# Performance work log

Hardware: AMD Instinct MI355X
Metric: run time of the kernel (lower is better)

The kernel has to match this reference:

```python
import jax, jax.numpy as jnp
import numpy as np

B, S, DM, H = 4, 1024, 1024, 16
D = DM // H  # head size 64


def setup_inputs() -> dict:
    key = jax.random.key(0)
    ks = jax.random.split(key, 8)
    scale = 1.0 / np.sqrt(DM)
    return {
        "hidden_states": jax.random.normal(ks[0], (B, S, DM), dtype=jnp.float32),
        "attention_mask": jnp.zeros((B, 1, 1, S), dtype=jnp.float32),
        "link_mask": jax.random.uniform(ks[1], (B, 1, S, S), dtype=jnp.float32),
        "Wq": jax.random.normal(ks[2], (DM, DM), dtype=jnp.float32) * scale,
        "bq": jnp.zeros((DM,), dtype=jnp.float32),
        "Wk": jax.random.normal(ks[3], (DM, DM), dtype=jnp.float32) * scale,
        "bk": jnp.zeros((DM,), dtype=jnp.float32),
        "Wv": jax.random.normal(ks[4], (DM, DM), dtype=jnp.float32) * scale,
        "bv": jnp.zeros((DM,), dtype=jnp.float32),
    }


def _split_heads(x):
    # [B,S,DM] -> [B,H,S,D]
    return x.reshape(B, S, H, D).transpose(0, 2, 1, 3)


def reference(hidden_states, attention_mask, link_mask, Wq, bq, Wk, bk, Wv, bv):
    q = _split_heads(hidden_states @ Wq.T + bq)
    k = _split_heads(hidden_states @ Wk.T + bk)
    v = _split_heads(hidden_states @ Wv.T + bv)
    # [B,H,S,S]
    scores = jnp.einsum("bhqd,bhkd->bhqk", q, k) / jnp.float32(np.sqrt(D))
    scores = scores + attention_mask  # additive mask, broadcast [B,1,1,S]
    probs = jax.nn.softmax(scores, axis=-1)
    # post-softmax multiplicative link mask (un-normalizes rows)
    probs = probs * link_mask
    # dropout prob 0.0 (eval) -> identity
    ctx = jnp.einsum("bhqk,bhkd->bhqd", probs, v)
    ctx = ctx.transpose(0, 2, 1, 3).reshape(B, S, DM)
    return ctx
```

## Files before the change

kernel.cpp:

```cpp
#include <hip/hip_runtime.h>
#include <hip/hip_bf16.h>
#include <cstdint>

typedef __attribute__((ext_vector_type(8))) __bf16 bf16x8;
typedef __attribute__((ext_vector_type(4))) float f32x4;
typedef unsigned short u16;
typedef unsigned int u32;

struct alignas(8) U16x4 { u16 x, y, z, w; };
struct alignas(8) U32x2 { u32 x, y; };

__device__ __forceinline__ u16 f2b(float x) {
    u32 u = __builtin_bit_cast(u32, x);
    u += 0x7fffu + ((u >> 16) & 1u);
    return (u16)(u >> 16);
}
__device__ __forceinline__ u32 cvtpk(float lo, float hi) {
    u32 r;
    asm("v_cvt_pk_bf16_f32 %0, %1, %2" : "=v"(r) : "v"(lo), "v"(hi));
    return r;
}
__device__ __forceinline__ float vexp2(float x) {
    float r;
    asm("v_exp_f32 %0, %1" : "=v"(r) : "v"(x));
    return r;
}

#define LOG2E 1.44269504088896f

__global__ __launch_bounds__(256) void cvt_kernel(
    const float* __restrict__ hs,
    const float* __restrict__ wq, const float* __restrict__ wk, const float* __restrict__ wv,
    const float* __restrict__ amask,
    u16* __restrict__ hsb, u16* __restrict__ wb, float* __restrict__ amask2)
{
    if (blockIdx.x == 7168) {
        int t = threadIdx.x;
        #pragma unroll
        for (int j = 0; j < 4; ++j) {
            float4 v = ((const float4*)amask)[t + j * 256];
            v.x *= LOG2E; v.y *= LOG2E; v.z *= LOG2E; v.w *= LOG2E;
            ((float4*)amask2)[t + j * 256] = v;
        }
        return;
    }
    int i = blockIdx.x * 256 + threadIdx.x;
    const float4* src; u16* dst; int off;
    if (i < 1048576) { src = (const float4*)hs; dst = hsb; off = i; }
    else {
        int j = i - 1048576;
        int w = j >> 18;
        int o = j & 262143;
        src = (const float4*)(w == 0 ? wq : (w == 1 ? wk : wv));
        dst = wb + w * 1048576;
        off = o;
    }
    float4 v = src[off];
    U16x4 r; r.x = f2b(v.x); r.y = f2b(v.y); r.z = f2b(v.z); r.w = f2b(v.w);
    *(U16x4*)(dst + off * 4) = r;
}

__global__ __launch_bounds__(256, 3) void qkv_gemm(
    const u16* __restrict__ A, const u16* __restrict__ W,
    const float* __restrict__ bq, const float* __restrict__ bk, const float* __restrict__ bv,
    u16* __restrict__ Qo, u16* __restrict__ Ko, u16* __restrict__ Vt)
{
    __shared__ u16 As[2][128 * 32];
    __shared__ u16 Bs[2][128 * 32];
    const int tid = threadIdx.x;
    const int lane = tid & 63, wid = tid >> 6;
    const int wr = (wid >> 1) * 64, wc = (wid & 1) * 64;
    const int g = lane >> 4, c = lane & 15;

    int lin = blockIdx.y * 24 + blockIdx.x;
    int wg = (lin & 7) * 96 + (lin >> 3);
    const int bn = wg >> 5;
    const int bm = wg & 31;

    f32x4 acc[4][4] = {};

#define GSTAGE(bf, k0)                                                              \
    {                                                                               \
        _Pragma("unroll") for (int i = 0; i < 2; ++i) {                             \
            int chunk = i * 256 + tid;                                              \
            int row = chunk >> 2, col = (chunk & 3) * 8;                            \
            const u16* ga = A + (bm * 128 + row) * 1024 + (k0) + col;               \
            const u16* gb = W + (bn * 128 + row) * 1024 + (k0) + col;               \
            u16* la = &As[bf][0] + (i * 256 + wid * 64) * 8;                        \
            u16* lb = &Bs[bf][0] + (i * 256 + wid * 64) * 8;                        \
            __builtin_amdgcn_global_load_lds((const __attribute__((address_space(1))) u32*)ga, \
                                             (__attribute__((address_space(3))) u32*)la, 16, 0, 0); \
            __builtin_amdgcn_global_load_lds((const __attribute__((address_space(1))) u32*)gb, \
                                             (__attribute__((address_space(3))) u32*)lb, 16, 0, 0); \
        }                                                                           \
    }

    GSTAGE(0, 0);

    int cur = 0;
    for (int t = 0; t < 32; ++t) {
        __syncthreads();
        if (t < 31) GSTAGE(cur ^ 1, (t + 1) * 32);
        bf16x8 af[4], bf4[4];
        #pragma unroll
        for (int i = 0; i < 4; ++i)
            af[i] = *(const bf16x8*)(&As[cur][0] + (wr + i * 16 + c) * 32 + g * 8);
        #pragma unroll
        for (int j = 0; j < 4; ++j)
            bf4[j] = *(const bf16x8*)(&Bs[cur][0] + (wc + j * 16 + c) * 32 + g * 8);
        #pragma unroll
        for (int i = 0; i < 4; ++i)
            #pragma unroll
            for (int j = 0; j < 4; ++j)
                acc[i][j] = __builtin_amdgcn_mfma_f32_16x16x32_bf16(af[i], bf4[j], acc[i][j], 0, 0, 0);
        cur ^= 1;
    }
#undef GSTAGE

    const int region = bn >> 3;
    const float* bias = region == 0 ? bq : (region == 1 ? bk : bv);
    #pragma unroll
    for (int i = 0; i < 4; ++i) {
        int m0 = bm * 128 + wr + i * 16 + g * 4;
        int b = m0 >> 10, s0 = m0 & 1023;
        #pragma unroll
        for (int j = 0; j < 4; ++j) {
            int n = (bn & 7) * 128 + wc + j * 16 + c;
            float bb = bias[n];
            int h = n >> 6, d = n & 63;
            int bh = b * 16 + h;
            if (region == 2) {
                U16x4 pk;
                pk.x = f2b(acc[i][j][0] + bb);
                pk.y = f2b(acc[i][j][1] + bb);
                pk.z = f2b(acc[i][j][2] + bb);
                pk.w = f2b(acc[i][j][3] + bb);
                *(U16x4*)(Vt + (bh * 64 + d) * 1024 + s0) = pk;
            } else if (region == 1) {
                #pragma unroll
                for (int r = 0; r < 4; ++r)
                    Ko[(bh * 1024 + s0 + r) * 64 + d] = f2b(acc[i][j][r] + bb);
            } else {
                #pragma unroll
                for (int r = 0; r < 4; ++r)
                    Qo[(bh * 1024 + s0 + r) * 64 + d] = f2b((acc[i][j][r] + bb) * (0.125f * LOG2E));
            }
        }
    }
}

__global__ __launch_bounds__(256, 4) void attn_kernel(
    const u16* __restrict__ Q, const u16* __restrict__ K, const u16* __restrict__ Vt,
    const float* __restrict__ amask, const float* __restrict__ link,
    float* __restrict__ out)
{
    __shared__ u16 Ks[2][32 * 64];
    __shared__ u16 Vs[2][64 * 32];
    __shared__ float Ls[2][64 * 32];
    __shared__ u16 P[4][16 * 32];
    const int tid = threadIdx.x;
    const int lane = tid & 63, wid = tid >> 6;
    const int g = lane >> 4, c = lane & 15;
    const int c7 = c & 7;
    const int s2 = (c >> 1) & 3;

    int hw = blockIdx.x;
    int logical = (hw & 7) * 128 + (hw >> 3);
    int b = logical >> 8;
    int qt = (logical >> 4) & 15;
    int h = logical & 15;
    int bh = b * 16 + h;
    const int qbase = qt * 64 + wid * 16;

    const u16* Qh = Q + bh * 65536;
    const u16* Kh = K + bh * 65536;
    const u16* Vh = Vt + bh * 65536;
    const float* Lq = link + (size_t)b * 1048576 + (size_t)(qt * 64) * 1024;

    bf16x8 qfx0 = *(const bf16x8*)(Qh + (qbase + c) * 64 + g * 8);
    bf16x8 qfx1 = *(const bf16x8*)(Qh + (qbase + c) * 64 + 32 + g * 8);

    float lsum = 0.f;
    f32x4 ctx[4] = {};
    u16* const Pb = &P[wid][0];

    const int krow = tid >> 3, kcir = (tid & 7) ^ (krow & 7);
    const int vrow = tid >> 2, vcir = (tid & 3) ^ ((vrow >> 1) & 3);
    const int lr1i = (256 + tid) >> 3;
    const int lc1 = ((256 + tid) & 7) ^ (lr1i & 7);
    const u16* gk   = Kh + krow * 64 + kcir * 8;
    const u16* gv   = Vh + vrow * 1024 + vcir * 8;
    const float* gl0 = Lq + krow * 1024 + kcir * 4;
    const float* gl1 = Lq + lr1i * 1024 + lc1 * 4;
    const float* mkP = amask + b * 1024;

#define AS3(p) (__attribute__((address_space(3))) u32*)(p)
#define AS1(p) (const __attribute__((address_space(1))) u32*)(p)
#define ISSUE_STAGE(B)                                                              \
    {                                                                               \
        __builtin_amdgcn_global_load_lds(AS1(gk),  AS3(&Ks[B][0] + wid * 512), 16, 0, 0); \
        __builtin_amdgcn_global_load_lds(AS1(gv),  AS3(&Vs[B][0] + wid * 512), 16, 0, 0); \
        __builtin_amdgcn_global_load_lds(AS1(gl0), AS3(&Ls[B][0] + wid * 256), 16, 0, 0); \
        __builtin_amdgcn_global_load_lds(AS1(gl1), AS3(&Ls[B][0] + 1024 + wid * 256), 16, 0, 0); \
        gk += 2048; gv += 32; gl0 += 32; gl1 += 32;                                 \
    }

#define ATILE(B, T)                                                                 \
    {                                                                               \
        __syncthreads();                 \
        if ((T) < 31) ISSUE_STAGE((B) ^ 1)                                          \
        _Pragma("unroll") for (int kt = 0; kt < 2; ++kt) {                          \
            bf16x8 kf0 = *(const bf16x8*)(&Ks[B][0] + (kt * 16 + c) * 64 + ((g)     ^ c7) * 8); \
            bf16x8 kf1 = *(const bf16x8*)(&Ks[B][0] + (kt * 16 + c) * 64 + ((4 + g) ^ c7) * 8); \
            f32x4 sc = {};                                                          \
            sc = __builtin_amdgcn_mfma_f32_16x16x32_bf16(kf0, qfx0, sc, 0, 0, 0);   \
            sc = __builtin_amdgcn_mfma_f32_16x16x32_bf16(kf1, qfx1, sc, 0, 0, 0);   \
            f32x4 m4  = *(const f32x4*)(mkP + kt * 16 + g * 4);                     \
            f32x4 lk4 = *(const f32x4*)(&Ls[B][0] + (wid * 16 + c) * 32 + ((kt * 4 + g) ^ c7) * 4); \
            float e0 = vexp2(sc[0] + m4[0]);                                        \
            float e1 = vexp2(sc[1] + m4[1]);                                        \
            float e2 = vexp2(sc[2] + m4[2]);                                        \
            float e3 = vexp2(sc[3] + m4[3]);                                        \
            lsum += (e0 + e1) + (e2 + e3);                                          \
            U32x2 pw;                                                               \
            pw.x = cvtpk(e0 * lk4[0], e1 * lk4[1]);                                 \
            pw.y = cvtpk(e2 * lk4[2], e3 * lk4[3]);                                 \
            *(U32x2*)(Pb + c * 32 + (((kt * 4 + g) ^ (s2 << 1)) * 4)) = pw;         \
        }                                                                           \
        __builtin_amdgcn_s_setprio(1);                                              \
        bf16x8 pf = *(const bf16x8*)(Pb + c * 32 + ((g ^ s2) * 8));                 \
        _Pragma("unroll") for (int dt = 0; dt < 4; ++dt) {                          \
            bf16x8 vf = *(const bf16x8*)(&Vs[B][0] + (dt * 16 + c) * 32 + ((g ^ s2) * 8)); \
            ctx[dt] = __builtin_amdgcn_mfma_f32_16x16x32_bf16(pf, vf, ctx[dt], 0, 0, 0); \
        }                                                                           \
        __builtin_amdgcn_s_setprio(0);                                              \
        mkP += 32;                                                                  \
    }

    ISSUE_STAGE(0)

    for (int it = 0; it < 16; ++it) {
        ATILE(0, it * 2);
        ATILE(1, it * 2 + 1);
    }
#undef ATILE
#undef ISSUE_STAGE
#undef AS3
#undef AS1

    lsum += __shfl_xor(lsum, 16, 64);
    lsum += __shfl_xor(lsum, 32, 64);

    #pragma unroll
    for (int r = 0; r < 4; ++r) {
        float inv = 1.0f / __shfl(lsum, g * 4 + r, 16);
        int q = qbase + g * 4 + r;
        float* orow = out + (size_t)b * 1048576 + (size_t)q * 1024 + h * 64;
        #pragma unroll
        for (int dt = 0; dt < 4; ++dt)
            orow[dt * 16 + c] = ctx[dt][r] * inv;
    }
}

extern "C" void kernel_launch(void* const* d_in, const int* in_sizes, int n_in,
                              void* d_out, int out_size, void* d_ws, size_t ws_size,
                              hipStream_t stream)
{
    (void)in_sizes; (void)n_in; (void)out_size; (void)ws_size;
    const float* hs    = (const float*)d_in[0];
    const float* amask = (const float*)d_in[1];
    const float* link  = (const float*)d_in[2];
    const float* Wq    = (const float*)d_in[3];
    const float* bq    = (const float*)d_in[4];
    const float* Wk    = (const float*)d_in[5];
    const float* bk    = (const float*)d_in[6];
    const float* Wv    = (const float*)d_in[7];
    const float* bv    = (const float*)d_in[8];
    float* out = (float*)d_out;

    char* ws = (char*)d_ws;
    u16* hsb = (u16*)ws;
    u16* wb  = (u16*)(ws + (8u  << 20));
    u16* Qb  = (u16*)(ws + (14u << 20));
    u16* Kb  = (u16*)(ws + (22u << 20));
    u16* Vtb = (u16*)(ws + (30u << 20));
    float* amask2 = (float*)(ws + (38u << 20));

    cvt_kernel<<<7169, 256, 0, stream>>>(hs, Wq, Wk, Wv, amask, hsb, wb, amask2);
    qkv_gemm<<<dim3(24, 32), 256, 0, stream>>>(hsb, wb, bq, bk, bv, Qb, Kb, Vtb);
    attn_kernel<<<1024, 256, 0, stream>>>(Qb, Kb, Vtb, amask2, link, out);
}
```

Before: 86.79 us.

## Switch attention to 32x32 MFMA tiles with register-resident P via permlane swap

The attention kernel now gives each wave 32 query rows instead of 16 and uses 32x32x16 bf16 MFMAs for both QK^T and PV. The probability tile is repacked in registers with v_permlane32_swap rather than round-tripping through LDS. This drops the P shared buffer and its LDS traffic, and the 32-row softmax sums reduce with a single shuffle. In exchange the block count halves to 512, occupancy drops to 2 blocks per CU, and each block stages twice as much link-mask data.

```diff
diff --git a/kernel.cpp b/kernel.cpp
--- a/kernel.cpp
+++ b/kernel.cpp
@@ -4,11 +4,12 @@
 
 typedef __attribute__((ext_vector_type(8))) __bf16 bf16x8;
 typedef __attribute__((ext_vector_type(4))) float f32x4;
+typedef __attribute__((ext_vector_type(16))) float f32x16;
 typedef unsigned short u16;
 typedef unsigned int u32;
 
 struct alignas(8) U16x4 { u16 x, y, z, w; };
-struct alignas(8) U32x2 { u32 x, y; };
+struct alignas(16) U32x4 { u32 x, y, z, w; };
 
 __device__ __forceinline__ u16 f2b(float x) {
     u32 u = __builtin_bit_cast(u32, x);
@@ -24,6 +25,9 @@
     float r;
     asm("v_exp_f32 %0, %1" : "=v"(r) : "v"(x));
     return r;
+}
+__device__ __forceinline__ void plswap(u32& a, u32& b) {
+    asm("v_permlane32_swap_b32 %0, %1" : "+v"(a), "+v"(b));
 }
 
 #define LOG2E 1.44269504088896f
@@ -149,50 +153,52 @@
     }
 }
 
-__global__ __launch_bounds__(256, 4) void attn_kernel(
+__global__ __launch_bounds__(256, 2) void attn_kernel(
     const u16* __restrict__ Q, const u16* __restrict__ K, const u16* __restrict__ Vt,
     const float* __restrict__ amask, const float* __restrict__ link,
     float* __restrict__ out)
 {
     __shared__ u16 Ks[2][32 * 64];
     __shared__ u16 Vs[2][64 * 32];
-    __shared__ float Ls[2][64 * 32];
-    __shared__ u16 P[4][16 * 32];
+    __shared__ float Ls[2][128 * 32];
     const int tid = threadIdx.x;
     const int lane = tid & 63, wid = tid >> 6;
-    const int g = lane >> 4, c = lane & 15;
-    const int c7 = c & 7;
-    const int s2 = (c >> 1) & 3;
+    const int c5 = lane & 31, hi = lane >> 5;
+    const int c7 = c5 & 7;
+    const int s2 = (c5 >> 1) & 3;
 
     int hw = blockIdx.x;
-    int logical = (hw & 7) * 128 + (hw >> 3);
-    int b = logical >> 8;
-    int qt = (logical >> 4) & 15;
+    int logical = (hw & 7) * 64 + (hw >> 3);
+    int b = logical >> 7;
+    int qt = (logical >> 4) & 7;
     int h = logical & 15;
     int bh = b * 16 + h;
-    const int qbase = qt * 64 + wid * 16;
+    const int qbase = qt * 128 + wid * 32;
 
     const u16* Qh = Q + bh * 65536;
     const u16* Kh = K + bh * 65536;
     const u16* Vh = Vt + bh * 65536;
-    const float* Lq = link + (size_t)b * 1048576 + (size_t)(qt * 64) * 1024;
-
-    bf16x8 qfx0 = *(const bf16x8*)(Qh + (qbase + c) * 64 + g * 8);
-    bf16x8 qfx1 = *(const bf16x8*)(Qh + (qbase + c) * 64 + 32 + g * 8);
+    const float* mkP = amask + b * 1024;
+    const float* Lq = link + (size_t)b * 1048576 + (size_t)(qt * 128) * 1024;
+
+    bf16x8 qf[4];
+    #pragma unroll
+    for (int m = 0; m < 4; ++m)
+        qf[m] = *(const bf16x8*)(Qh + (qbase + c5) * 64 + m * 16 + hi * 8);
 
     float lsum = 0.f;
-    f32x4 ctx[4] = {};
-    u16* const Pb = &P[wid][0];
-
-    const int krow = tid >> 3, kcir = (tid & 7) ^ (krow & 7);
-    const int vrow = tid >> 2, vcir = (tid & 3) ^ ((vrow >> 1) & 3);
-    const int lr1i = (256 + tid) >> 3;
-    const int lc1 = ((256 + tid) & 7) ^ (lr1i & 7);
-    const u16* gk   = Kh + krow * 64 + kcir * 8;
-    const u16* gv   = Vh + vrow * 1024 + vcir * 8;
-    const float* gl0 = Lq + krow * 1024 + kcir * 4;
-    const float* gl1 = Lq + lr1i * 1024 + lc1 * 4;
-    const float* mkP = amask + b * 1024;
+    f32x16 ctx0 = {}, ctx1 = {};
+
+    const int krow = tid >> 3;
+    const int vrow = tid >> 2;
+    const int lrow = tid >> 3;
+    const u16* gk  = Kh + krow * 64 + (((tid & 7) ^ (krow & 7)) * 8);
+    const u16* gv  = Vh + vrow * 1024 + (((tid & 3) ^ ((vrow >> 1) & 3)) * 8);
+    const int lcir = (tid & 7) ^ (lrow & 7);
+    const float* gl0 = Lq + (lrow +  0) * 1024 + lcir * 4;
+    const float* gl1 = Lq + (lrow + 32) * 1024 + lcir * 4;
+    const float* gl2 = Lq + (lrow + 64) * 1024 + lcir * 4;
+    const float* gl3 = Lq + (lrow + 96) * 1024 + lcir * 4;
 
 #define AS3(p) (__attribute__((address_space(3))) u32*)(p)
 #define AS1(p) (const __attribute__((address_space(1))) u32*)(p)
@@ -200,38 +206,51 @@
     {                                                                               \
         __builtin_amdgcn_global_load_lds(AS1(gk),  AS3(&Ks[B][0] + wid * 512), 16, 0, 0); \
         __builtin_amdgcn_global_load_lds(AS1(gv),  AS3(&Vs[B][0] + wid * 512), 16, 0, 0); \
-        __builtin_amdgcn_global_load_lds(AS1(gl0), AS3(&Ls[B][0] + wid * 256), 16, 0, 0); \
+        __builtin_amdgcn_global_load_lds(AS1(gl0), AS3(&Ls[B][0] +        wid * 256), 16, 0, 0); \
         __builtin_amdgcn_global_load_lds(AS1(gl1), AS3(&Ls[B][0] + 1024 + wid * 256), 16, 0, 0); \
-        gk += 2048; gv += 32; gl0 += 32; gl1 += 32;                                 \
+        __builtin_amdgcn_global_load_lds(AS1(gl2), AS3(&Ls[B][0] + 2048 + wid * 256), 16, 0, 0); \
+        __builtin_amdgcn_global_load_lds(AS1(gl3), AS3(&Ls[B][0] + 3072 + wid * 256), 16, 0, 0); \
+        gk += 2048; gv += 32; gl0 += 32; gl1 += 32; gl2 += 32; gl3 += 32;           \
     }
 
 #define ATILE(B, T)                                                                 \
     {                                                                               \
         __syncthreads();                 \
         if ((T) < 31) ISSUE_STAGE((B) ^ 1)                                          \
-        _Pragma("unroll") for (int kt = 0; kt < 2; ++kt) {                          \
-            bf16x8 kf0 = *(const bf16x8*)(&Ks[B][0] + (kt * 16 + c) * 64 + ((g)     ^ c7) * 8); \
-            bf16x8 kf1 = *(const bf16x8*)(&Ks[B][0] + (kt * 16 + c) * 64 + ((4 + g) ^ c7) * 8); \
-            f32x4 sc = {};                                                          \
-            sc = __builtin_amdgcn_mfma_f32_16x16x32_bf16(kf0, qfx0, sc, 0, 0, 0);   \
-            sc = __builtin_amdgcn_mfma_f32_16x16x32_bf16(kf1, qfx1, sc, 0, 0, 0);   \
-            f32x4 m4  = *(const f32x4*)(mkP + kt * 16 + g * 4);                     \
-            f32x4 lk4 = *(const f32x4*)(&Ls[B][0] + (wid * 16 + c) * 32 + ((kt * 4 + g) ^ c7) * 4); \
-            float e0 = vexp2(sc[0] + m4[0]);                                        \
-            float e1 = vexp2(sc[1] + m4[1]);                                        \
-            float e2 = vexp2(sc[2] + m4[2]);                                        \
-            float e3 = vexp2(sc[3] + m4[3]);                                        \
-            lsum += (e0 + e1) + (e2 + e3);                                          \
-            U32x2 pw;                                                               \
-            pw.x = cvtpk(e0 * lk4[0], e1 * lk4[1]);                                 \
-            pw.y = cvtpk(e2 * lk4[2], e3 * lk4[3]);                                 \
-            *(U32x2*)(Pb + c * 32 + (((kt * 4 + g) ^ (s2 << 1)) * 4)) = pw;         \
-        }                                                                           \
+        f32x16 sc = {};                                                             \
+        _Pragma("unroll") for (int m = 0; m < 4; ++m) {                             \
+            bf16x8 kf = *(const bf16x8*)(&Ks[B][0] + c5 * 64 + (((2 * m + hi) ^ c7) * 8)); \
+            sc = __builtin_amdgcn_mfma_f32_32x32x16_bf16(kf, qf[m], sc, 0, 0, 0);   \
+        }                                                                           \
+        f32x4 mq[4], lq[4];                                                         \
+        _Pragma("unroll") for (int j = 0; j < 4; ++j) {                             \
+            mq[j] = *(const f32x4*)(mkP + j * 8 + hi * 4);                          \
+            lq[j] = *(const f32x4*)(&Ls[B][0] + (wid * 32 + c5) * 32 + (((2 * j + hi) ^ c7) * 4)); \
+        }                                                                           \
+        float p[16];                                                                \
+        _Pragma("unroll") for (int r = 0; r < 16; ++r) {                            \
+            float e = vexp2(sc[r] + mq[r >> 2][r & 3]);                             \
+            lsum += e;                                                              \
+            p[r] = e * lq[r >> 2][r & 3];                                           \
+        }                                                                           \
+        u32 a0 = cvtpk(p[0], p[1]),   b0 = cvtpk(p[4], p[5]);                       \
+        u32 a1 = cvtpk(p[2], p[3]),   b1 = cvtpk(p[6], p[7]);                       \
+        u32 a2 = cvtpk(p[8], p[9]),   b2 = cvtpk(p[12], p[13]);                     \
+        u32 a3 = cvtpk(p[10], p[11]), b3 = cvtpk(p[14], p[15]);                     \
+        plswap(a0, b0); plswap(a1, b1); plswap(a2, b2); plswap(a3, b3);             \
+        U32x4 w0 = {a0, a1, b0, b1}, w1 = {a2, a3, b2, b3};                         \
+        bf16x8 pa0 = __builtin_bit_cast(bf16x8, w0);           \
+        bf16x8 pa1 = __builtin_bit_cast(bf16x8, w1);           \
         __builtin_amdgcn_s_setprio(1);                                              \
-        bf16x8 pf = *(const bf16x8*)(Pb + c * 32 + ((g ^ s2) * 8));                 \
-        _Pragma("unroll") for (int dt = 0; dt < 4; ++dt) {                          \
-            bf16x8 vf = *(const bf16x8*)(&Vs[B][0] + (dt * 16 + c) * 32 + ((g ^ s2) * 8)); \
-            ctx[dt] = __builtin_amdgcn_mfma_f32_16x16x32_bf16(pf, vf, ctx[dt], 0, 0, 0); \
+        {                                                                           \
+            bf16x8 v00 = *(const bf16x8*)(&Vs[B][0] + c5 * 32 + (((0 + hi) ^ s2) * 8)); \
+            bf16x8 v01 = *(const bf16x8*)(&Vs[B][0] + c5 * 32 + (((2 + hi) ^ s2) * 8)); \
+            bf16x8 v10 = *(const bf16x8*)(&Vs[B][0] + (32 + c5) * 32 + (((0 + hi) ^ s2) * 8)); \
+            bf16x8 v11 = *(const bf16x8*)(&Vs[B][0] + (32 + c5) * 32 + (((2 + hi) ^ s2) * 8)); \
+            ctx0 = __builtin_amdgcn_mfma_f32_32x32x16_bf16(v00, pa0, ctx0, 0, 0, 0); \
+            ctx1 = __builtin_amdgcn_mfma_f32_32x32x16_bf16(v10, pa0, ctx1, 0, 0, 0); \
+            ctx0 = __builtin_amdgcn_mfma_f32_32x32x16_bf16(v01, pa1, ctx0, 0, 0, 0); \
+            ctx1 = __builtin_amdgcn_mfma_f32_32x32x16_bf16(v11, pa1, ctx1, 0, 0, 0); \
         }                                                                           \
         __builtin_amdgcn_s_setprio(0);                                              \
         mkP += 32;                                                                  \
@@ -248,17 +267,18 @@
 #undef AS3
 #undef AS1
 
-    lsum += __shfl_xor(lsum, 16, 64);
     lsum += __shfl_xor(lsum, 32, 64);
-
+    float inv = 1.0f / lsum;
+
+    float* orow = out + (size_t)b * 1048576 + (size_t)(qbase + c5) * 1024 + h * 64;
     #pragma unroll
-    for (int r = 0; r < 4; ++r) {
-        float inv = 1.0f / __shfl(lsum, g * 4 + r, 16);
-        int q = qbase + g * 4 + r;
-        float* orow = out + (size_t)b * 1048576 + (size_t)q * 1024 + h * 64;
-        #pragma unroll
-        for (int dt = 0; dt < 4; ++dt)
-            orow[dt * 16 + c] = ctx[dt][r] * inv;
+    for (int rq = 0; rq < 4; ++rq) {
+        f32x4 o0 = { ctx0[rq * 4 + 0] * inv, ctx0[rq * 4 + 1] * inv,
+                     ctx0[rq * 4 + 2] * inv, ctx0[rq * 4 + 3] * inv };
+        f32x4 o1 = { ctx1[rq * 4 + 0] * inv, ctx1[rq * 4 + 1] * inv,
+                     ctx1[rq * 4 + 2] * inv, ctx1[rq * 4 + 3] * inv };
+        *(f32x4*)(orow + rq * 8 + hi * 4)      = o0;
+        *(f32x4*)(orow + 32 + rq * 8 + hi * 4) = o1;
     }
 }
 
@@ -288,5 +308,5 @@
 
     cvt_kernel<<<7169, 256, 0, stream>>>(hs, Wq, Wk, Wv, amask, hsb, wb, amask2);
     qkv_gemm<<<dim3(24, 32), 256, 0, stream>>>(hsb, wb, bq, bk, bv, Qb, Kb, Vtb);
-    attn_kernel<<<1024, 256, 0, stream>>>(Qb, Kb, Vtb, amask2, link, out);
-}
+    attn_kernel<<<512, 256, 0, stream>>>(Qb, Kb, Vtb, amask2, link, out);
+}
```

Result: no change. 86.37 us (-0.5%).

## Double attention query tile per block to reuse K/V tiles across 32 rows per wave

Applied to the files above, without the earlier changes.

Each wave now handles 32 query rows instead of 16, so every block covers 128 queries and the grid shrinks from 1024 to 512 blocks. Each K and V tile loaded into shared memory now feeds twice as many MFMAs, which halves K/V global and LDS traffic per query. The link-mask staging buffer and P scratch double in size and the launch bound drops to 2 blocks per CU. The cost is higher register and LDS pressure, lower occupancy, and fewer blocks to spread across the CUs.

```diff
diff --git a/kernel.cpp b/kernel.cpp
--- a/kernel.cpp
+++ b/kernel.cpp
@@ -149,15 +149,15 @@
     }
 }
 
-__global__ __launch_bounds__(256, 4) void attn_kernel(
+__global__ __launch_bounds__(256, 2) void attn_kernel(
     const u16* __restrict__ Q, const u16* __restrict__ K, const u16* __restrict__ Vt,
     const float* __restrict__ amask, const float* __restrict__ link,
     float* __restrict__ out)
 {
     __shared__ u16 Ks[2][32 * 64];
     __shared__ u16 Vs[2][64 * 32];
-    __shared__ float Ls[2][64 * 32];
-    __shared__ u16 P[4][16 * 32];
+    __shared__ float Ls[2][128 * 32];
+    __shared__ u16 P[4][32 * 32];
     const int tid = threadIdx.x;
     const int lane = tid & 63, wid = tid >> 6;
     const int g = lane >> 4, c = lane & 15;
@@ -165,33 +165,37 @@
     const int s2 = (c >> 1) & 3;
 
     int hw = blockIdx.x;
-    int logical = (hw & 7) * 128 + (hw >> 3);
-    int b = logical >> 8;
-    int qt = (logical >> 4) & 15;
+    int logical = (hw & 7) * 64 + (hw >> 3);
+    int b = logical >> 7;
+    int qt = (logical >> 4) & 7;
     int h = logical & 15;
     int bh = b * 16 + h;
-    const int qbase = qt * 64 + wid * 16;
+    const int qbase = qt * 128 + wid * 32;
 
     const u16* Qh = Q + bh * 65536;
     const u16* Kh = K + bh * 65536;
     const u16* Vh = Vt + bh * 65536;
-    const float* Lq = link + (size_t)b * 1048576 + (size_t)(qt * 64) * 1024;
-
-    bf16x8 qfx0 = *(const bf16x8*)(Qh + (qbase + c) * 64 + g * 8);
-    bf16x8 qfx1 = *(const bf16x8*)(Qh + (qbase + c) * 64 + 32 + g * 8);
-
-    float lsum = 0.f;
-    f32x4 ctx[4] = {};
+    const float* Lq = link + (size_t)b * 1048576 + (size_t)(qt * 128) * 1024;
+
+    bf16x8 qf00 = *(const bf16x8*)(Qh + (qbase + c) * 64 + g * 8);
+    bf16x8 qf01 = *(const bf16x8*)(Qh + (qbase + c) * 64 + 32 + g * 8);
+    bf16x8 qf10 = *(const bf16x8*)(Qh + (qbase + 16 + c) * 64 + g * 8);
+    bf16x8 qf11 = *(const bf16x8*)(Qh + (qbase + 16 + c) * 64 + 32 + g * 8);
+
+    float lsum0 = 0.f, lsum1 = 0.f;
+    f32x4 ctx0[4] = {}, ctx1[4] = {};
     u16* const Pb = &P[wid][0];
 
     const int krow = tid >> 3, kcir = (tid & 7) ^ (krow & 7);
     const int vrow = tid >> 2, vcir = (tid & 3) ^ ((vrow >> 1) & 3);
-    const int lr1i = (256 + tid) >> 3;
-    const int lc1 = ((256 + tid) & 7) ^ (lr1i & 7);
+    const int lrow = tid >> 3;
+    const int lcir = (tid & 7) ^ (lrow & 7);
     const u16* gk   = Kh + krow * 64 + kcir * 8;
     const u16* gv   = Vh + vrow * 1024 + vcir * 8;
-    const float* gl0 = Lq + krow * 1024 + kcir * 4;
-    const float* gl1 = Lq + lr1i * 1024 + lc1 * 4;
+    const float* gl0 = Lq + (lrow +  0) * 1024 + lcir * 4;
+    const float* gl1 = Lq + (lrow + 32) * 1024 + lcir * 4;
+    const float* gl2 = Lq + (lrow + 64) * 1024 + lcir * 4;
+    const float* gl3 = Lq + (lrow + 96) * 1024 + lcir * 4;
     const float* mkP = amask + b * 1024;
 
 #define AS3(p) (__attribute__((address_space(3))) u32*)(p)
@@ -200,9 +204,11 @@
     {                                                                               \
         __builtin_amdgcn_global_load_lds(AS1(gk),  AS3(&Ks[B][0] + wid * 512), 16, 0, 0); \
         __builtin_amdgcn_global_load_lds(AS1(gv),  AS3(&Vs[B][0] + wid * 512), 16, 0, 0); \
-        __builtin_amdgcn_global_load_lds(AS1(gl0), AS3(&Ls[B][0] + wid * 256), 16, 0, 0); \
+        __builtin_amdgcn_global_load_lds(AS1(gl0), AS3(&Ls[B][0] +        wid * 256), 16, 0, 0); \
         __builtin_amdgcn_global_load_lds(AS1(gl1), AS3(&Ls[B][0] + 1024 + wid * 256), 16, 0, 0); \
-        gk += 2048; gv += 32; gl0 += 32; gl1 += 32;                                 \
+        __builtin_amdgcn_global_load_lds(AS1(gl2), AS3(&Ls[B][0] + 2048 + wid * 256), 16, 0, 0); \
+        __builtin_amdgcn_global_load_lds(AS1(gl3), AS3(&Ls[B][0] + 3072 + wid * 256), 16, 0, 0); \
+        gk += 2048; gv += 32; gl0 += 32; gl1 += 32; gl2 += 32; gl3 += 32;           \
     }
 
 #define ATILE(B, T)                                                                 \
@@ -212,26 +218,46 @@
         _Pragma("unroll") for (int kt = 0; kt < 2; ++kt) {                          \
             bf16x8 kf0 = *(const bf16x8*)(&Ks[B][0] + (kt * 16 + c) * 64 + ((g)     ^ c7) * 8); \
             bf16x8 kf1 = *(const bf16x8*)(&Ks[B][0] + (kt * 16 + c) * 64 + ((4 + g) ^ c7) * 8); \
-            f32x4 sc = {};                                                          \
-            sc = __builtin_amdgcn_mfma_f32_16x16x32_bf16(kf0, qfx0, sc, 0, 0, 0);   \
-            sc = __builtin_amdgcn_mfma_f32_16x16x32_bf16(kf1, qfx1, sc, 0, 0, 0);   \
-            f32x4 m4  = *(const f32x4*)(mkP + kt * 16 + g * 4);                     \
-            f32x4 lk4 = *(const f32x4*)(&Ls[B][0] + (wid * 16 + c) * 32 + ((kt * 4 + g) ^ c7) * 4); \
-            float e0 = vexp2(sc[0] + m4[0]);                                        \
-            float e1 = vexp2(sc[1] + m4[1]);                                        \
-            float e2 = vexp2(sc[2] + m4[2]);                                        \
-            float e3 = vexp2(sc[3] + m4[3]);                                        \
-            lsum += (e0 + e1) + (e2 + e3);                                          \
-            U32x2 pw;                                                               \
-            pw.x = cvtpk(e0 * lk4[0], e1 * lk4[1]);                                 \
-            pw.y = cvtpk(e2 * lk4[2], e3 * lk4[3]);                                 \
-            *(U32x2*)(Pb + c * 32 + (((kt * 4 + g) ^ (s2 << 1)) * 4)) = pw;         \
+            f32x4 sc0 = {}, sc1 = {};                                               \
+            sc0 = __builtin_amdgcn_mfma_f32_16x16x32_bf16(kf0, qf00, sc0, 0, 0, 0); \
+            sc0 = __builtin_amdgcn_mfma_f32_16x16x32_bf16(kf1, qf01, sc0, 0, 0, 0); \
+            sc1 = __builtin_amdgcn_mfma_f32_16x16x32_bf16(kf0, qf10, sc1, 0, 0, 0); \
+            sc1 = __builtin_amdgcn_mfma_f32_16x16x32_bf16(kf1, qf11, sc1, 0, 0, 0); \
+            f32x4 m4 = *(const f32x4*)(mkP + kt * 16 + g * 4);                      \
+            {                                                           \
+                f32x4 lk4 = *(const f32x4*)(&Ls[B][0] + (wid * 32 + c) * 32 + ((kt * 4 + g) ^ c7) * 4); \
+                float e0 = vexp2(sc0[0] + m4[0]);                                   \
+                float e1 = vexp2(sc0[1] + m4[1]);                                   \
+                float e2 = vexp2(sc0[2] + m4[2]);                                   \
+                float e3 = vexp2(sc0[3] + m4[3]);                                   \
+                lsum0 += (e0 + e1) + (e2 + e3);                                     \
+                U32x2 pw;                                                           \
+                pw.x = cvtpk(e0 * lk4[0], e1 * lk4[1]);                             \
+                pw.y = cvtpk(e2 * lk4[2], e3 * lk4[3]);                             \
+                *(U32x2*)(Pb + c * 32 + (((kt * 4 + g) ^ (s2 << 1)) * 4)) = pw;     \
+            }                                                                       \
+            {                                                           \
+                f32x4 lk4 = *(const f32x4*)(&Ls[B][0] + (wid * 32 + 16 + c) * 32 + ((kt * 4 + g) ^ c7) * 4); \
+                float e0 = vexp2(sc1[0] + m4[0]);                                   \
+                float e1 = vexp2(sc1[1] + m4[1]);                                   \
+                float e2 = vexp2(sc1[2] + m4[2]);                                   \
+                float e3 = vexp2(sc1[3] + m4[3]);                                   \
+                lsum1 += (e0 + e1) + (e2 + e3);                                     \
+                U32x2 pw;                                                           \
+                pw.x = cvtpk(e0 * lk4[0], e1 * lk4[1]);                             \
+                pw.y = cvtpk(e2 * lk4[2], e3 * lk4[3]);                             \
+                *(U32x2*)(Pb + (16 + c) * 32 + (((kt * 4 + g) ^ (s2 << 1)) * 4)) = pw; \
+            }                                                                       \
         }                                                                           \
         __builtin_amdgcn_s_setprio(1);                                              \
-        bf16x8 pf = *(const bf16x8*)(Pb + c * 32 + ((g ^ s2) * 8));                 \
-        _Pragma("unroll") for (int dt = 0; dt < 4; ++dt) {                          \
-            bf16x8 vf = *(const bf16x8*)(&Vs[B][0] + (dt * 16 + c) * 32 + ((g ^ s2) * 8)); \
-            ctx[dt] = __builtin_amdgcn_mfma_f32_16x16x32_bf16(pf, vf, ctx[dt], 0, 0, 0); \
+        {                                                                           \
+            bf16x8 pf0 = *(const bf16x8*)(Pb + c * 32 + ((g ^ s2) * 8));            \
+            bf16x8 pf1 = *(const bf16x8*)(Pb + (16 + c) * 32 + ((g ^ s2) * 8));     \
+            _Pragma("unroll") for (int dt = 0; dt < 4; ++dt) {                      \
+                bf16x8 vf = *(const bf16x8*)(&Vs[B][0] + (dt * 16 + c) * 32 + ((g ^ s2) * 8)); \
+                ctx0[dt] = __builtin_amdgcn_mfma_f32_16x16x32_bf16(pf0, vf, ctx0[dt], 0, 0, 0); \
+                ctx1[dt] = __builtin_amdgcn_mfma_f32_16x16x32_bf16(pf1, vf, ctx1[dt], 0, 0, 0); \
+            }                                                                       \
         }                                                                           \
         __builtin_amdgcn_s_setprio(0);                                              \
         mkP += 32;                                                                  \
@@ -248,17 +274,23 @@
 #undef AS3
 #undef AS1
 
-    lsum += __shfl_xor(lsum, 16, 64);
-    lsum += __shfl_xor(lsum, 32, 64);
+    lsum0 += __shfl_xor(lsum0, 16, 64);
+    lsum0 += __shfl_xor(lsum0, 32, 64);
+    lsum1 += __shfl_xor(lsum1, 16, 64);
+    lsum1 += __shfl_xor(lsum1, 32, 64);
 
     #pragma unroll
     for (int r = 0; r < 4; ++r) {
-        float inv = 1.0f / __shfl(lsum, g * 4 + r, 16);
-        int q = qbase + g * 4 + r;
-        float* orow = out + (size_t)b * 1048576 + (size_t)q * 1024 + h * 64;
-        #pragma unroll
-        for (int dt = 0; dt < 4; ++dt)
-            orow[dt * 16 + c] = ctx[dt][r] * inv;
+        float inv0 = 1.0f / __shfl(lsum0, g * 4 + r, 16);
+        float inv1 = 1.0f / __shfl(lsum1, g * 4 + r, 16);
+        int q0 = qbase + g * 4 + r;
+        float* orow0 = out + (size_t)b * 1048576 + (size_t)q0 * 1024 + h * 64;
+        float* orow1 = orow0 + 16 * 1024;
+        #pragma unroll
+        for (int dt = 0; dt < 4; ++dt) {
+            orow0[dt * 16 + c] = ctx0[dt][r] * inv0;
+            orow1[dt * 16 + c] = ctx1[dt][r] * inv1;
+        }
     }
 }
 
@@ -288,5 +320,5 @@
 
     cvt_kernel<<<7169, 256, 0, stream>>>(hs, Wq, Wk, Wv, amask, hsb, wb, amask2);
     qkv_gemm<<<dim3(24, 32), 256, 0, stream>>>(hsb, wb, bq, bk, bv, Qb, Kb, Vtb);
-    attn_kernel<<<1024, 256, 0, stream>>>(Qb, Kb, Vtb, amask2, link, out);
-}
+    attn_kernel<<<512, 256, 0, stream>>>(Qb, Kb, Vtb, amask2, link, out);
+}
```

Result: no change. 86.68 us (-0.1%).

## Pre-convert link mask to permuted bf16 and stream it into attention

Applied to the files above, without the earlier changes.

Adds a pass to the conversion kernel that turns the fp32 link mask into bf16. The pass also permutes each 32-column block to match the fragment order the attention kernel reads. The attention kernel then loads half as many link bytes per tile, with one async LDS copy instead of two, and unpacks bf16 pairs with shifts and masks. The cost being targeted is the repeated per-head reads of the full-precision link mask through cache and LDS. In exchange it adds an extra write and read of the converted buffer per call and rounds the mask to bf16 before the multiply.

```diff
diff --git a/kernel.cpp b/kernel.cpp
--- a/kernel.cpp
+++ b/kernel.cpp
@@ -9,6 +9,7 @@
 
 struct alignas(8) U16x4 { u16 x, y, z, w; };
 struct alignas(8) U32x2 { u32 x, y; };
+struct alignas(16) U32x4 { u32 x, y, z, w; };
 
 __device__ __forceinline__ u16 f2b(float x) {
     u32 u = __builtin_bit_cast(u32, x);
@@ -25,14 +26,19 @@
     asm("v_exp_f32 %0, %1" : "=v"(r) : "v"(x));
     return r;
 }
+__device__ __forceinline__ float blo(u32 w) { return __builtin_bit_cast(float, w << 16); }
+__device__ __forceinline__ float bhi(u32 w) { return __builtin_bit_cast(float, w & 0xffff0000u); }
 
 #define LOG2E 1.44269504088896f
+#define AS3(p) (__attribute__((address_space(3))) u32*)(p)
+#define AS1(p) (const __attribute__((address_space(1))) u32*)(p)
 
 __global__ __launch_bounds__(256) void cvt_kernel(
     const float* __restrict__ hs,
     const float* __restrict__ wq, const float* __restrict__ wk, const float* __restrict__ wv,
-    const float* __restrict__ amask,
-    u16* __restrict__ hsb, u16* __restrict__ wb, float* __restrict__ amask2)
+    const float* __restrict__ amask, const float* __restrict__ link,
+    u16* __restrict__ hsb, u16* __restrict__ wb, float* __restrict__ amask2,
+    u16* __restrict__ linkb)
 {
     if (blockIdx.x == 7168) {
         int t = threadIdx.x;
@@ -42,6 +48,17 @@
             v.x *= LOG2E; v.y *= LOG2E; v.z *= LOG2E; v.w *= LOG2E;
             ((float4*)amask2)[t + j * 256] = v;
         }
+        return;
+    }
+    if (blockIdx.x > 7168) {
+        int chunk = (blockIdx.x - 7169) * 256 + threadIdx.x;
+        float4 v = ((const float4*)link)[chunk];
+        int row = chunk >> 8;
+        int k4 = chunk & 255;
+        int blk = k4 >> 3, k4in = k4 & 7;
+        int newu = ((k4in & 3) << 1) | (k4in >> 2);
+        U16x4 r4; r4.x = f2b(v.x); r4.y = f2b(v.y); r4.z = f2b(v.z); r4.w = f2b(v.w);
+        *(U16x4*)(linkb + row * 1024 + blk * 32 + newu * 4) = r4;
         return;
     }
     int i = blockIdx.x * 256 + threadIdx.x;
@@ -88,10 +105,8 @@
             const u16* gb = W + (bn * 128 + row) * 1024 + (k0) + col;               \
             u16* la = &As[bf][0] + (i * 256 + wid * 64) * 8;                        \
             u16* lb = &Bs[bf][0] + (i * 256 + wid * 64) * 8;                        \
-            __builtin_amdgcn_global_load_lds((const __attribute__((address_space(1))) u32*)ga, \
-                                             (__attribute__((address_space(3))) u32*)la, 16, 0, 0); \
-            __builtin_amdgcn_global_load_lds((const __attribute__((address_space(1))) u32*)gb, \
-                                             (__attribute__((address_space(3))) u32*)lb, 16, 0, 0); \
+            __builtin_amdgcn_global_load_lds(AS1(ga), AS3(la), 16, 0, 0);           \
+            __builtin_amdgcn_global_load_lds(AS1(gb), AS3(lb), 16, 0, 0);           \
         }                                                                           \
     }
 
@@ -151,12 +166,12 @@
 
 __global__ __launch_bounds__(256, 4) void attn_kernel(
     const u16* __restrict__ Q, const u16* __restrict__ K, const u16* __restrict__ Vt,
-    const float* __restrict__ amask, const float* __restrict__ link,
+    const float* __restrict__ amask, const u16* __restrict__ linkb,
     float* __restrict__ out)
 {
     __shared__ u16 Ks[2][32 * 64];
     __shared__ u16 Vs[2][64 * 32];
-    __shared__ float Ls[2][64 * 32];
+    __shared__ u16 Ls[2][64 * 32];
     __shared__ u16 P[4][16 * 32];
     const int tid = threadIdx.x;
     const int lane = tid & 63, wid = tid >> 6;
@@ -175,7 +190,6 @@
     const u16* Qh = Q + bh * 65536;
     const u16* Kh = K + bh * 65536;
     const u16* Vh = Vt + bh * 65536;
-    const float* Lq = link + (size_t)b * 1048576 + (size_t)(qt * 64) * 1024;
 
     bf16x8 qfx0 = *(const bf16x8*)(Qh + (qbase + c) * 64 + g * 8);
     bf16x8 qfx1 = *(const bf16x8*)(Qh + (qbase + c) * 64 + 32 + g * 8);
@@ -186,45 +200,43 @@
 
     const int krow = tid >> 3, kcir = (tid & 7) ^ (krow & 7);
     const int vrow = tid >> 2, vcir = (tid & 3) ^ ((vrow >> 1) & 3);
-    const int lr1i = (256 + tid) >> 3;
-    const int lc1 = ((256 + tid) & 7) ^ (lr1i & 7);
-    const u16* gk   = Kh + krow * 64 + kcir * 8;
-    const u16* gv   = Vh + vrow * 1024 + vcir * 8;
-    const float* gl0 = Lq + krow * 1024 + kcir * 4;
-    const float* gl1 = Lq + lr1i * 1024 + lc1 * 4;
+    const u16* gk = Kh + krow * 64 + kcir * 8;
+    const u16* gv = Vh + vrow * 1024 + vcir * 8;
+    const u16* gl = linkb + (size_t)b * 1048576
+                    + (size_t)(qt * 64 + (tid >> 2)) * 1024 + (tid & 3) * 8;
     const float* mkP = amask + b * 1024;
 
-#define AS3(p) (__attribute__((address_space(3))) u32*)(p)
-#define AS1(p) (const __attribute__((address_space(1))) u32*)(p)
 #define ISSUE_STAGE(B)                                                              \
     {                                                                               \
-        __builtin_amdgcn_global_load_lds(AS1(gk),  AS3(&Ks[B][0] + wid * 512), 16, 0, 0); \
-        __builtin_amdgcn_global_load_lds(AS1(gv),  AS3(&Vs[B][0] + wid * 512), 16, 0, 0); \
-        __builtin_amdgcn_global_load_lds(AS1(gl0), AS3(&Ls[B][0] + wid * 256), 16, 0, 0); \
-        __builtin_amdgcn_global_load_lds(AS1(gl1), AS3(&Ls[B][0] + 1024 + wid * 256), 16, 0, 0); \
-        gk += 2048; gv += 32; gl0 += 32; gl1 += 32;                                 \
+        __builtin_amdgcn_global_load_lds(AS1(gk), AS3(&Ks[B][0] + wid * 512), 16, 0, 0); \
+        __builtin_amdgcn_global_load_lds(AS1(gv), AS3(&Vs[B][0] + wid * 512), 16, 0, 0); \
+        __builtin_amdgcn_global_load_lds(AS1(gl), AS3(&Ls[B][0] + wid * 512), 16, 0, 0); \
+        gk += 2048; gv += 32; gl += 32;                                             \
     }
 
 #define ATILE(B, T)                                                                 \
     {                                                                               \
         __syncthreads();                 \
         if ((T) < 31) ISSUE_STAGE((B) ^ 1)                                          \
+        bf16x8 lk8 = *(const bf16x8*)(&Ls[B][0] + (wid * 16 + c) * 32 + g * 8);     \
+        U32x4 lw = __builtin_bit_cast(U32x4, lk8);                                  \
         _Pragma("unroll") for (int kt = 0; kt < 2; ++kt) {                          \
             bf16x8 kf0 = *(const bf16x8*)(&Ks[B][0] + (kt * 16 + c) * 64 + ((g)     ^ c7) * 8); \
             bf16x8 kf1 = *(const bf16x8*)(&Ks[B][0] + (kt * 16 + c) * 64 + ((4 + g) ^ c7) * 8); \
             f32x4 sc = {};                                                          \
             sc = __builtin_amdgcn_mfma_f32_16x16x32_bf16(kf0, qfx0, sc, 0, 0, 0);   \
             sc = __builtin_amdgcn_mfma_f32_16x16x32_bf16(kf1, qfx1, sc, 0, 0, 0);   \
-            f32x4 m4  = *(const f32x4*)(mkP + kt * 16 + g * 4);                     \
-            f32x4 lk4 = *(const f32x4*)(&Ls[B][0] + (wid * 16 + c) * 32 + ((kt * 4 + g) ^ c7) * 4); \
+            f32x4 m4 = *(const f32x4*)(mkP + kt * 16 + g * 4);                      \
             float e0 = vexp2(sc[0] + m4[0]);                                        \
             float e1 = vexp2(sc[1] + m4[1]);                                        \
             float e2 = vexp2(sc[2] + m4[2]);                                        \
             float e3 = vexp2(sc[3] + m4[3]);                                        \
             lsum += (e0 + e1) + (e2 + e3);                                          \
+            u32 wa  = kt ? lw.z : lw.x;                                             \
+            u32 wbq = kt ? lw.w : lw.y;                                             \
             U32x2 pw;                                                               \
-            pw.x = cvtpk(e0 * lk4[0], e1 * lk4[1]);                                 \
-            pw.y = cvtpk(e2 * lk4[2], e3 * lk4[3]);                                 \
+            pw.x = cvtpk(e0 * blo(wa),  e1 * bhi(wa));                              \
+            pw.y = cvtpk(e2 * blo(wbq), e3 * bhi(wbq));                             \
             *(U32x2*)(Pb + c * 32 + (((kt * 4 + g) ^ (s2 << 1)) * 4)) = pw;         \
         }                                                                           \
         __builtin_amdgcn_s_setprio(1);                                              \
@@ -245,8 +257,6 @@
     }
 #undef ATILE
 #undef ISSUE_STAGE
-#undef AS3
-#undef AS1
 
     lsum += __shfl_xor(lsum, 16, 64);
     lsum += __shfl_xor(lsum, 32, 64);
@@ -285,8 +295,9 @@
     u16* Kb  = (u16*)(ws + (22u << 20));
     u16* Vtb = (u16*)(ws + (30u << 20));
     float* amask2 = (float*)(ws + (38u << 20));
-
-    cvt_kernel<<<7169, 256, 0, stream>>>(hs, Wq, Wk, Wv, amask, hsb, wb, amask2);
+    u16* linkb = (u16*)(ws + (40u << 20));
+
+    cvt_kernel<<<11265, 256, 0, stream>>>(hs, Wq, Wk, Wv, amask, link, hsb, wb, amask2, linkb);
     qkv_gemm<<<dim3(24, 32), 256, 0, stream>>>(hsb, wb, bq, bk, bv, Qb, Kb, Vtb);
-    attn_kernel<<<1024, 256, 0, stream>>>(Qb, Kb, Vtb, amask2, link, out);
-}
+    attn_kernel<<<1024, 256, 0, stream>>>(Qb, Kb, Vtb, amask2, linkb, out);
+}
```

Measured after the change: 88.49 us. About the same (+2.0%).
